# Kernel tuning notes

Hardware: AMD Instinct MI355X
Metric: run time of the kernel (lower is better)

Reference implementation:

```python
import jax, jax.numpy as jnp
import numpy as np

N_NODES = 100000


def setup_inputs() -> dict:
    key = jax.random.key(0)
    ks = jax.random.split(key, 11)
    d_in, d_out = 64, 64
    n_edges = 1600000
    x = jax.random.normal(ks[0], (N_NODES, d_in), dtype=jnp.float32)
    edge_index = jax.random.randint(ks[1], (2, n_edges), 0, N_NODES, dtype=jnp.int64)
    s = 1.0 / np.sqrt(d_in)
    return {
        "x": x,
        "edge_index": edge_index,
        "W_key": jax.random.normal(ks[2], (d_in, d_out), dtype=jnp.float32) * s,
        "b_key": jax.random.normal(ks[3], (d_out,), dtype=jnp.float32) * s,
        "W_query": jax.random.normal(ks[4], (d_in, d_out), dtype=jnp.float32) * s,
        "b_query": jax.random.normal(ks[5], (d_out,), dtype=jnp.float32) * s,
        "W_value": jax.random.normal(ks[6], (d_in, d_out), dtype=jnp.float32) * s,
        "b_value": jax.random.normal(ks[7], (d_out,), dtype=jnp.float32) * s,
        "W_skip": jax.random.normal(ks[8], (d_in, d_out), dtype=jnp.float32) * s,
        "b_skip": jax.random.normal(ks[9], (d_out,), dtype=jnp.float32) * s,
    }


def reference(x, edge_index, W_key, b_key, W_query, b_query, W_value, b_value, W_skip, b_skip):
    # ResGatedGraphConv: out_i = W_skip x_i + sum_{j->i} sigmoid(k_i + q_j) * v_j
    k = x @ W_key + b_key      # [N, d_out], keyed by target node i
    q = x @ W_query + b_query  # [N, d_out], keyed by source node j
    v = x @ W_value + b_value  # [N, d_out]
    src = edge_index[0]  # j (message source)
    dst = edge_index[1]  # i (aggregation target)
    gate = jax.nn.sigmoid(k[dst] + q[src])  # [E, d_out]
    msg = gate * v[src]                     # [E, d_out]
    agg = jax.ops.segment_sum(msg, dst, num_segments=N_NODES)
    return agg + x @ W_skip + b_skip
```

## Files before the change

kernel.cpp:

```cpp
#include <hip/hip_runtime.h>
#include <hip/hip_bf16.h>
#include <cstdint>

#define NPB 32
#define CHUNK 8192
#define CAP1 73728
#define CAP2 1216
#define NCOARSE 25
#define NFINEREG 1600
#define WPC 9

__device__ inline unsigned int bf16_rne(float f) {
    unsigned int b = __float_as_uint(f);
    b += 0x7FFFu + ((b >> 16) & 1u);
    return b >> 16;
}

__global__ __launch_bounds__(256) void fused_linear_kernel(
    const float* __restrict__ x,
    const float* __restrict__ Wk, const float* __restrict__ bk,
    const float* __restrict__ Wq, const float* __restrict__ bq,
    const float* __restrict__ Wv, const float* __restrict__ bv,
    const float* __restrict__ Ws, const float* __restrict__ bs,
    float* __restrict__ karr, unsigned int* __restrict__ qvp,
    float* __restrict__ out, int N)
{
    __shared__ float sW[4][64][64];
    __shared__ float sb[4][64];
    __shared__ float sx[NPB][64];

    const int tid = threadIdx.x;

    const float* Wsrc[4] = {Wk, Wq, Wv, Ws};
    const float* bsrc[4] = {bk, bq, bv, bs};
    #pragma unroll
    for (int m = 0; m < 4; ++m) {
        const float4* src = (const float4*)Wsrc[m];
        float4* dstp = (float4*)&sW[m][0][0];
        for (int i = tid; i < 1024; i += 256) dstp[i] = src[i];
        if (tid < 64) sb[m][tid] = bsrc[m][tid];
    }

    const int node0 = blockIdx.x * NPB;
    {
        const float4* xs = (const float4*)(x + (size_t)node0 * 64);
        float4* xd = (float4*)&sx[0][0];
        int cnt = NPB * 16;
        int maxv = (N - node0) * 16;
        if (maxv > cnt) maxv = cnt;
        for (int i = tid; i < cnt; i += 256)
            xd[i] = (i < maxv) ? xs[i] : float4{0.f, 0.f, 0.f, 0.f};
    }
    __syncthreads();

    const int w = tid >> 6;
    const int l = tid & 63;
    const int nbase = w * 8;

    float acc[8][4];
    #pragma unroll
    for (int r = 0; r < 8; ++r)
        #pragma unroll
        for (int m = 0; m < 4; ++m) acc[r][m] = 0.f;

    #pragma unroll 16
    for (int i = 0; i < 64; ++i) {
        float wv4[4];
        #pragma unroll
        for (int m = 0; m < 4; ++m) wv4[m] = sW[m][i][l];
        #pragma unroll
        for (int r = 0; r < 8; ++r) {
            float xb = sx[nbase + r][i];
            #pragma unroll
            for (int m = 0; m < 4; ++m) acc[r][m] = fmaf(xb, wv4[m], acc[r][m]);
        }
    }

    #pragma unroll
    for (int r = 0; r < 8; ++r) {
        int node = node0 + nbase + r;
        if (node < N) {
            karr[(size_t)node * 64 + l] = acc[r][0] + sb[0][l];
            unsigned int qb = bf16_rne(acc[r][1] + sb[1][l]);
            unsigned int vb = bf16_rne(acc[r][2] + sb[2][l]);
            qvp[(size_t)node * 64 + l] = qb | (vb << 16);
            out[(size_t)node * 64 + l] = acc[r][3] + sb[3][l];
        }
    }
}

__global__ __launch_bounds__(256) void bin1_kernel(
    const int* __restrict__ esrc, const int* __restrict__ edst,
    unsigned int* __restrict__ pairs1, int* __restrict__ gcur1, int E)
{
    __shared__ unsigned int stage[CHUNK];
    __shared__ unsigned char bstage[CHUNK];
    __shared__ int hist[32], lofs[32], fragbase[32], lcur[32];

    const int t = threadIdx.x;
    if (t < 32) hist[t] = 0;
    __syncthreads();

    const int base = blockIdx.x * CHUNK;
    const int cnt = min(CHUNK, E - base);

    for (int i = t; i < cnt; i += 256) {
        int d = edst[base + i];
        atomicAdd(&hist[d >> 12], 1);
    }
    __syncthreads();

    if (t < NCOARSE) {
        int h = hist[t];
        fragbase[t] = h ? atomicAdd(&gcur1[t], h) : 0;
        lcur[t] = 0;
    }
    if (t == 0) {
        int run = 0;
        for (int b = 0; b < NCOARSE; ++b) { lofs[b] = run; run += hist[b]; }
    }
    __syncthreads();

    for (int i = t; i < cnt; i += 256) {
        int d = edst[base + i];
        int s = esrc[base + i];
        int b = d >> 12;
        int r = atomicAdd(&lcur[b], 1);
        int p = lofs[b] + r;
        stage[p] = ((unsigned int)(d & 4095) << 17) | (unsigned int)s;
        bstage[p] = (unsigned char)b;
    }
    __syncthreads();

    for (int i = t; i < cnt; i += 256) {
        int b = bstage[i];
        int gpos = fragbase[b] + (i - lofs[b]);
        if (gpos < CAP1)
            pairs1[(size_t)b * CAP1 + gpos] = stage[i];
    }
}

__global__ __launch_bounds__(256) void bin2_kernel(
    const unsigned int* __restrict__ pairs1, const int* __restrict__ gcur1,
    unsigned int* __restrict__ packed2, int* __restrict__ gcur2)
{
    __shared__ unsigned int stage[CHUNK];
    __shared__ unsigned char bstage[CHUNK];
    __shared__ int hist[64], lofs[64], fragbase[64], lcur[64];

    const int c   = blockIdx.x / WPC;
    const int sub = blockIdx.x % WPC;
    const int total = min(gcur1[c], CAP1);
    const int base = sub * CHUNK;
    if (base >= total) return;
    const int cnt = min(CHUNK, total - base);
    const int t = threadIdx.x;

    if (t < 64) hist[t] = 0;
    __syncthreads();

    const unsigned int* src = pairs1 + (size_t)c * CAP1 + base;

    for (int i = t; i < cnt; i += 256) {
        unsigned int pv = src[i];
        atomicAdd(&hist[(pv >> 17) >> 6], 1);
    }
    __syncthreads();

    if (t < 64) {
        int h = hist[t];
        fragbase[t] = h ? atomicAdd(&gcur2[(c << 6) + t], h) : 0;
        lcur[t] = 0;
    }
    if (t == 0) {
        int run = 0;
        for (int b = 0; b < 64; ++b) { lofs[b] = run; run += hist[b]; }
    }
    __syncthreads();

    for (int i = t; i < cnt; i += 256) {
        unsigned int pv = src[i];
        int dl12 = pv >> 17;
        int f = dl12 >> 6;
        int r = atomicAdd(&lcur[f], 1);
        int p = lofs[f] + r;
        stage[p] = ((unsigned int)(dl12 & 63) << 17) | (pv & 0x1FFFFu);
        bstage[p] = (unsigned char)f;
    }
    __syncthreads();

    for (int i = t; i < cnt; i += 256) {
        int f = bstage[i];
        int gpos = fragbase[f] + (i - lofs[f]);
        if (gpos < CAP2)
            packed2[(size_t)((c << 6) + f) * CAP2 + gpos] = stage[i];
    }
}

__global__ __launch_bounds__(256) void bin3_kernel(
    const unsigned int* __restrict__ packed2, const int* __restrict__ gcur2,
    unsigned int* __restrict__ packed3, int* __restrict__ nstart,
    int* __restrict__ ncnt)
{
    const int fg = blockIdx.x;
    const int cnt = min(gcur2[fg], CAP2);
    const int t = threadIdx.x;

    __shared__ int hist[64], offs[64], cur[64];
    if (t < 64) hist[t] = 0;
    __syncthreads();

    const unsigned int* src = packed2 + (size_t)fg * CAP2;

    for (int i = t; i < cnt; i += 256)
        atomicAdd(&hist[src[i] >> 17], 1);
    __syncthreads();

    if (t == 0) {
        int run = 0;
        for (int b = 0; b < 64; ++b) { offs[b] = run; cur[b] = run; run += hist[b]; }
    }
    __syncthreads();

    if (t < 64) {
        nstart[(fg << 6) + t] = fg * CAP2 + offs[t];
        ncnt[(fg << 6) + t]   = hist[t];
    }

    for (int i = t; i < cnt; i += 256) {
        unsigned int pv = src[i];
        int dl = pv >> 17;
        int p = atomicAdd(&cur[dl], 1);
        packed3[(size_t)fg * CAP2 + p] = pv & 0x1FFFFu;
    }
}

__global__ __launch_bounds__(256) void agg_kernel(
    const unsigned int* __restrict__ packed3,
    const int* __restrict__ nstart, const int* __restrict__ ncnt,
    const float* __restrict__ karr, const unsigned int* __restrict__ qvp,
    float* __restrict__ out, int N)
{
    const int node = blockIdx.x * 4 + (threadIdx.x >> 6);
    if (node >= N) return;
    const int lane = threadIdx.x & 63;

    const int start = nstart[node];
    const int cnt   = ncnt[node];

    const float kv = karr[(size_t)node * 64 + lane];
    float acc = 0.f;

    for (int base = 0; base < cnt; base += 64) {
        const int c = min(64, cnt - base);
        const int sid = (base + lane < cnt) ? (int)packed3[start + base + lane] : 0;
        int i = 0;
        for (; i + 1 < c; i += 2) {
            int s0 = __shfl(sid, i);
            int s1 = __shfl(sid, i + 1);
            unsigned int u0 = qvp[(size_t)s0 * 64 + lane];
            unsigned int u1 = qvp[(size_t)s1 * 64 + lane];
            float q0 = __uint_as_float(u0 << 16);
            float v0 = __uint_as_float(u0 & 0xFFFF0000u);
            float q1 = __uint_as_float(u1 << 16);
            float v1 = __uint_as_float(u1 & 0xFFFF0000u);
            acc += v0 / (1.f + __expf(-(kv + q0)));
            acc += v1 / (1.f + __expf(-(kv + q1)));
        }
        if (i < c) {
            int s0 = __shfl(sid, i);
            unsigned int u0 = qvp[(size_t)s0 * 64 + lane];
            float q0 = __uint_as_float(u0 << 16);
            float v0 = __uint_as_float(u0 & 0xFFFF0000u);
            acc += v0 / (1.f + __expf(-(kv + q0)));
        }
    }

    out[(size_t)node * 64 + lane] += acc;
}

extern "C" void kernel_launch(void* const* d_in, const int* in_sizes, int n_in,
                              void* d_out, int out_size, void* d_ws, size_t ws_size,
                              hipStream_t stream) {
    const float* x  = (const float*)d_in[0];
    const int* edge = (const int*)d_in[1];
    const float* Wk = (const float*)d_in[2];
    const float* bk = (const float*)d_in[3];
    const float* Wq = (const float*)d_in[4];
    const float* bq = (const float*)d_in[5];
    const float* Wv = (const float*)d_in[6];
    const float* bv = (const float*)d_in[7];
    const float* Ws = (const float*)d_in[8];
    const float* bs = (const float*)d_in[9];
    float* out = (float*)d_out;

    const int N = in_sizes[0] / 64;
    const int E = in_sizes[1] / 2;
    const int* esrc = edge;
    const int* edst = edge + E;

    char* ws = (char*)d_ws;
    float* karr  = (float*)ws;                  ws += (size_t)N * 64 * 4;
    unsigned int* qvp = (unsigned int*)ws;      ws += (size_t)N * 64 * 4;
    unsigned int* packed2 = (unsigned int*)ws;  ws += (size_t)NFINEREG * CAP2 * 4;
    unsigned int* packed3 = (unsigned int*)ws;  ws += (size_t)NFINEREG * CAP2 * 4;
    int* nstart = (int*)ws;                     ws += (size_t)NFINEREG * 64 * 4;
    int* ncnt   = (int*)ws;                     ws += (size_t)NFINEREG * 64 * 4;
    int* gcur1  = (int*)ws;                     ws += 32 * 4;
    int* gcur2  = (int*)ws;                     ws += (size_t)NFINEREG * 4;
    unsigned int* pairs1 = (unsigned int*)karr;

    hipMemsetAsync(gcur1, 0, (32 + NFINEREG) * 4, stream);

    const int nb1 = (E + CHUNK - 1) / CHUNK;
    bin1_kernel<<<nb1, 256, 0, stream>>>(esrc, edst, pairs1, gcur1, E);
    bin2_kernel<<<NCOARSE * WPC, 256, 0, stream>>>(pairs1, gcur1, packed2, gcur2);
    bin3_kernel<<<NFINEREG, 256, 0, stream>>>(packed2, gcur2, packed3, nstart, ncnt);

    const int nblocks1 = (N + NPB - 1) / NPB;
    fused_linear_kernel<<<nblocks1, 256, 0, stream>>>(
        x, Wk, bk, Wq, bq, Wv, bv, Ws, bs, karr, qvp, out, N);

    const int ablocks = (N + 3) / 4;
    agg_kernel<<<ablocks, 256, 0, stream>>>(packed3, nstart, ncnt, karr, qvp, out, N);
}
```

Before: 300.3 us.

## Fuse final binning pass into aggregation kernel using shared-memory edge lists

Merges the bin3 fine-binning kernel into the aggregation kernel. Each 1024-thread block now sorts its 64-node region's edges by destination in LDS, with a wave-level prefix scan for offsets, and then aggregates those nodes directly. This removes the packed3/nstart/ncnt global round trip and one kernel launch. The sigmoid now uses exp2 and a hardware reciprocal instead of a divide, and the edge loop is unrolled by four. The cost is fewer, larger blocks (1600 of them) with 16 waves each handling four nodes in sequence, which can hurt load balance and occupancy.

```diff
diff --git a/kernel.cpp b/kernel.cpp
--- a/kernel.cpp
+++ b/kernel.cpp
@@ -9,6 +9,7 @@
 #define NCOARSE 25
 #define NFINEREG 1600
 #define WPC 9
+#define LOG2E 1.44269504f
 
 __device__ inline unsigned int bf16_rne(float f) {
     unsigned int b = __float_as_uint(f);
@@ -197,86 +198,92 @@
     }
 }
 
-__global__ __launch_bounds__(256) void bin3_kernel(
+__global__ __launch_bounds__(1024) void agg_kernel(
     const unsigned int* __restrict__ packed2, const int* __restrict__ gcur2,
-    unsigned int* __restrict__ packed3, int* __restrict__ nstart,
-    int* __restrict__ ncnt)
+    const float* __restrict__ karr, const unsigned int* __restrict__ qvp,
+    float* __restrict__ out, int N)
 {
     const int fg = blockIdx.x;
+    const int node0 = fg << 6;
+    if (node0 >= N) return;
     const int cnt = min(gcur2[fg], CAP2);
     const int t = threadIdx.x;
 
-    __shared__ int hist[64], offs[64], cur[64];
+    __shared__ unsigned int sed[CAP2];
+    __shared__ int hist[64], nst[65], cur[64];
+
     if (t < 64) hist[t] = 0;
     __syncthreads();
 
     const unsigned int* src = packed2 + (size_t)fg * CAP2;
 
-    for (int i = t; i < cnt; i += 256)
+    for (int i = t; i < cnt; i += 1024)
         atomicAdd(&hist[src[i] >> 17], 1);
     __syncthreads();
 
-    if (t == 0) {
-        int run = 0;
-        for (int b = 0; b < 64; ++b) { offs[b] = run; cur[b] = run; run += hist[b]; }
-    }
-    __syncthreads();
-
     if (t < 64) {
-        nstart[(fg << 6) + t] = fg * CAP2 + offs[t];
-        ncnt[(fg << 6) + t]   = hist[t];
-    }
-
-    for (int i = t; i < cnt; i += 256) {
+        int v = hist[t];
+        int x = v;
+        #pragma unroll
+        for (int d = 1; d < 64; d <<= 1) {
+            int y = __shfl_up(x, d);
+            if (t >= d) x += y;
+        }
+        nst[t] = x - v;
+        cur[t] = x - v;
+        if (t == 63) nst[64] = x;
+    }
+    __syncthreads();
+
+    for (int i = t; i < cnt; i += 1024) {
         unsigned int pv = src[i];
         int dl = pv >> 17;
         int p = atomicAdd(&cur[dl], 1);
-        packed3[(size_t)fg * CAP2 + p] = pv & 0x1FFFFu;
-    }
-}
-
-__global__ __launch_bounds__(256) void agg_kernel(
-    const unsigned int* __restrict__ packed3,
-    const int* __restrict__ nstart, const int* __restrict__ ncnt,
-    const float* __restrict__ karr, const unsigned int* __restrict__ qvp,
-    float* __restrict__ out, int N)
-{
-    const int node = blockIdx.x * 4 + (threadIdx.x >> 6);
-    if (node >= N) return;
-    const int lane = threadIdx.x & 63;
-
-    const int start = nstart[node];
-    const int cnt   = ncnt[node];
-
-    const float kv = karr[(size_t)node * 64 + lane];
-    float acc = 0.f;
-
-    for (int base = 0; base < cnt; base += 64) {
-        const int c = min(64, cnt - base);
-        const int sid = (base + lane < cnt) ? (int)packed3[start + base + lane] : 0;
-        int i = 0;
-        for (; i + 1 < c; i += 2) {
-            int s0 = __shfl(sid, i);
-            int s1 = __shfl(sid, i + 1);
-            unsigned int u0 = qvp[(size_t)s0 * 64 + lane];
-            unsigned int u1 = qvp[(size_t)s1 * 64 + lane];
-            float q0 = __uint_as_float(u0 << 16);
-            float v0 = __uint_as_float(u0 & 0xFFFF0000u);
-            float q1 = __uint_as_float(u1 << 16);
-            float v1 = __uint_as_float(u1 & 0xFFFF0000u);
-            acc += v0 / (1.f + __expf(-(kv + q0)));
-            acc += v1 / (1.f + __expf(-(kv + q1)));
-        }
-        if (i < c) {
-            int s0 = __shfl(sid, i);
-            unsigned int u0 = qvp[(size_t)s0 * 64 + lane];
-            float q0 = __uint_as_float(u0 << 16);
-            float v0 = __uint_as_float(u0 & 0xFFFF0000u);
-            acc += v0 / (1.f + __expf(-(kv + q0)));
-        }
-    }
-
-    out[(size_t)node * 64 + lane] += acc;
+        sed[p] = pv & 0x1FFFFu;
+    }
+    __syncthreads();
+
+    const int w = t >> 6;
+    const int lane = t & 63;
+
+    for (int nl = w; nl < 64; nl += 16) {
+        const int node = node0 + nl;
+        if (node >= N) continue;
+
+        const float kv  = karr[(size_t)node * 64 + lane];
+        const float kvc = kv * -LOG2E;
+        float acc = 0.f;
+
+        const int s0i = nst[nl], e0i = nst[nl + 1];
+        int i = s0i;
+        for (; i + 3 < e0i; i += 4) {
+            int sa = (int)sed[i], sb2 = (int)sed[i + 1];
+            int sc = (int)sed[i + 2], sd = (int)sed[i + 3];
+            unsigned int ua = qvp[(size_t)sa * 64 + lane];
+            unsigned int ub = qvp[(size_t)sb2 * 64 + lane];
+            unsigned int uc = qvp[(size_t)sc * 64 + lane];
+            unsigned int ud = qvp[(size_t)sd * 64 + lane];
+            #pragma unroll
+            for (int j = 0; j < 4; ++j) {
+                unsigned int u = (j == 0) ? ua : (j == 1) ? ub : (j == 2) ? uc : ud;
+                float q = __uint_as_float(u << 16);
+                float v = __uint_as_float(u & 0xFFFF0000u);
+                float e = __builtin_amdgcn_exp2f(fmaf(q, -LOG2E, kvc));
+                float r = __builtin_amdgcn_rcpf(1.f + e);
+                acc = fmaf(v, r, acc);
+            }
+        }
+        for (; i < e0i; ++i) {
+            unsigned int u = qvp[(size_t)sed[i] * 64 + lane];
+            float q = __uint_as_float(u << 16);
+            float v = __uint_as_float(u & 0xFFFF0000u);
+            float e = __builtin_amdgcn_exp2f(fmaf(q, -LOG2E, kvc));
+            float r = __builtin_amdgcn_rcpf(1.f + e);
+            acc = fmaf(v, r, acc);
+        }
+
+        out[(size_t)node * 64 + lane] += acc;
+    }
 }
 
 extern "C" void kernel_launch(void* const* d_in, const int* in_sizes, int n_in,
@@ -303,9 +310,6 @@
     float* karr  = (float*)ws;                  ws += (size_t)N * 64 * 4;
     unsigned int* qvp = (unsigned int*)ws;      ws += (size_t)N * 64 * 4;
     unsigned int* packed2 = (unsigned int*)ws;  ws += (size_t)NFINEREG * CAP2 * 4;
-    unsigned int* packed3 = (unsigned int*)ws;  ws += (size_t)NFINEREG * CAP2 * 4;
-    int* nstart = (int*)ws;                     ws += (size_t)NFINEREG * 64 * 4;
-    int* ncnt   = (int*)ws;                     ws += (size_t)NFINEREG * 64 * 4;
     int* gcur1  = (int*)ws;                     ws += 32 * 4;
     int* gcur2  = (int*)ws;                     ws += (size_t)NFINEREG * 4;
     unsigned int* pairs1 = (unsigned int*)karr;
@@ -315,12 +319,10 @@
     const int nb1 = (E + CHUNK - 1) / CHUNK;
     bin1_kernel<<<nb1, 256, 0, stream>>>(esrc, edst, pairs1, gcur1, E);
     bin2_kernel<<<NCOARSE * WPC, 256, 0, stream>>>(pairs1, gcur1, packed2, gcur2);
-    bin3_kernel<<<NFINEREG, 256, 0, stream>>>(packed2, gcur2, packed3, nstart, ncnt);
 
     const int nblocks1 = (N + NPB - 1) / NPB;
     fused_linear_kernel<<<nblocks1, 256, 0, stream>>>(
         x, Wk, bk, Wq, bq, Wv, bv, Ws, bs, karr, qvp, out, N);
 
-    const int ablocks = (N + 3) / 4;
-    agg_kernel<<<ablocks, 256, 0, stream>>>(packed3, nstart, ncnt, karr, qvp, out, N);
-}
+    agg_kernel<<<NFINEREG, 1024, 0, stream>>>(packed2, gcur2, karr, qvp, out, N);
+}
```

After: 283.2 us. 5.7% less time.
